# Kernel optimization log

Measured on AMD Instinct MI355X. Metric: run time of the kernel, lower is better.

## Reference

```python
import jax, jax.numpy as jnp
import numpy as np

B, H, N, M, C = 64, 8, 16384, 64, 1024
IVH = 3 * M + 6  # per-head interface size: k(M), beta, g, s(3), gamma, e(M), a(M)


def setup_inputs() -> dict:
    key = jax.random.key(0)
    k1, k2, k3, k4 = jax.random.split(key, 4)
    return {
        "x": jax.random.normal(k1, (B, C), dtype=jnp.float32),
        "current_memory": jax.random.normal(k2, (B, N, M), dtype=jnp.float32),
        "w_prev": jax.random.uniform(k3, (B, H, N), dtype=jnp.float32),
        "W": jax.random.normal(k4, (C, H * IVH), dtype=jnp.float32) * (1.0 / np.sqrt(C)),
        "b": jnp.zeros((H * IVH,), dtype=jnp.float32),
    }


def reference(x, current_memory, w_prev, W, b):
    eps = 1e-16
    iv = (x @ W + b).reshape(B, H, IVH)
    k = iv[..., :M]                                   # [B,H,M] content key
    beta = jax.nn.softplus(iv[..., M])                # [B,H] key strength
    g = jax.nn.sigmoid(iv[..., M + 1])                # [B,H] interpolation gate
    s = jax.nn.softmax(iv[..., M + 2:M + 5], axis=-1) # [B,H,3] shift weights
    gamma = 1.0 + jax.nn.softplus(iv[..., M + 5])     # [B,H] sharpening
    e = jax.nn.sigmoid(iv[..., M + 6:2 * M + 6])      # [B,H,M] erase
    a = iv[..., 2 * M + 6:3 * M + 6]                  # [B,H,M] add

    # content addressing: cosine similarity of k against every memory row
    num = jnp.einsum('bhm,bnm->bhn', k, current_memory)
    den = (jnp.linalg.norm(k, axis=-1)[..., None]
           * jnp.linalg.norm(current_memory, axis=-1)[:, None, :] + eps)
    cos = num / den                                   # [B,H,N]
    wc = jax.nn.softmax(beta[..., None] * cos, axis=-1)

    # gated interpolation with previous weighting
    wg = g[..., None] * wc + (1.0 - g[..., None]) * w_prev

    # circular conv1d shift with 3-tap kernel (shifts -1, 0, +1)
    ws = (s[..., 0:1] * jnp.roll(wg, 1, axis=-1)
          + s[..., 1:2] * wg
          + s[..., 2:3] * jnp.roll(wg, -1, axis=-1))

    # sharpening (power normalize)
    wp = ws ** gamma[..., None]
    w = wp / (jnp.sum(wp, axis=-1, keepdims=True) + eps)

    # read
    read_data = jnp.einsum('bhn,bnm->bhm', w, current_memory)
    return (read_data, w, e, a)
```

## Files before the change

### kernel.cpp

```cpp
#include <hip/hip_runtime.h>
#include <cstdint>
#include <cstddef>

#define B_    64
#define H_    8
#define N_    16384
#define M_    64
#define C_    1024
#define IVH_  198
#define J_    1584
#define NCHUNK_ 64

__device__ __forceinline__ float softplus_f(float x) {
    return (x > 20.f) ? x : log1pf(__expf(x));
}
__device__ __forceinline__ float sigmoid_f(float x) {
    return 1.f / (1.f + __expf(-x));
}

__global__ __launch_bounds__(64) void k_gemm(const float* __restrict__ x,
                                             const float* __restrict__ W,
                                             float* __restrict__ iv) {
    int lane = threadIdx.x;
    int j = blockIdx.x * 64 + lane;
    bool valid = (j < J_);
    int b0 = blockIdx.y * 16;
    int c0 = blockIdx.z * 128;
    const float* xb = x + (size_t)b0 * C_;
    float acc[16];
    #pragma unroll
    for (int i = 0; i < 16; ++i) acc[i] = 0.f;
    #pragma unroll 2
    for (int c = c0; c < c0 + 128; ++c) {
        float wv = valid ? W[(size_t)c * J_ + j] : 0.f;
        #pragma unroll
        for (int bi = 0; bi < 16; ++bi)
            acc[bi] = fmaf(xb[(size_t)bi * C_ + c], wv, acc[bi]);
    }
    if (valid) {
        #pragma unroll
        for (int bi = 0; bi < 16; ++bi)
            atomicAdd(&iv[(size_t)(b0 + bi) * J_ + j], acc[bi]);
    }
}

__global__ void k_params(const float* __restrict__ iv, const float* __restrict__ bias,
                         float* __restrict__ kbuf, float* __restrict__ P,
                         float* __restrict__ out_e, float* __restrict__ out_a) {
    int bh = blockIdx.x;
    int m  = threadIdx.x;
    int b = bh >> 3, h = bh & 7;
    const float* row = iv + (size_t)b * J_ + h * IVH_;
    const float* bb  = bias + h * IVH_;
    float kv = row[m] + bb[m];
    kbuf[(size_t)bh * 64 + m] = kv;
    float s = kv * kv;
    #pragma unroll
    for (int o = 32; o > 0; o >>= 1) s += __shfl_down(s, o, 64);
    float ev = row[70 + m] + bb[70 + m];
    out_e[(size_t)bh * 64 + m] = sigmoid_f(ev);
    out_a[(size_t)bh * 64 + m] = row[134 + m] + bb[134 + m];
    if (m == 0) {
        float knorm = sqrtf(s);
        float v0 = row[64] + bb[64];
        float v1 = row[65] + bb[65];
        float v2 = row[66] + bb[66];
        float v3 = row[67] + bb[67];
        float v4 = row[68] + bb[68];
        float v5 = row[69] + bb[69];
        float beta = softplus_f(v0);
        float g = sigmoid_f(v1);
        float mx = fmaxf(v2, fmaxf(v3, v4));
        float e2 = __expf(v2 - mx), e3 = __expf(v3 - mx), e4 = __expf(v4 - mx);
        float inv = 1.f / (e2 + e3 + e4);
        float gamma = 1.f + softplus_f(v5);
        float* p = P + (size_t)bh * 8;
        p[0] = knorm; p[1] = beta; p[2] = g;
        p[3] = e2 * inv; p[4] = e3 * inv; p[5] = e4 * inv;
        p[6] = gamma;
    }
}

__global__ __launch_bounds__(256, 4) void k_passA(
        const float* __restrict__ mem, const float* __restrict__ kbuf,
        const float* __restrict__ P, float* __restrict__ z,
        float* __restrict__ pmax, float* __restrict__ psum) {
    __shared__ float zl[8 * 257];
    int t = threadIdx.x;
    int b = blockIdx.y;
    int n0 = blockIdx.x << 8;
    int w = t >> 6, lane = t & 63, sub = lane >> 4, mq = lane & 15;

    float4 kreg[8];
    #pragma unroll
    for (int h = 0; h < 8; ++h)
        kreg[h] = *(const float4*)(kbuf + (((size_t)b * 8 + h) << 6) + mq * 4);
    float beta = 0.f, knorm = 1.f;
    if (mq < 8) {
        const float* p = P + (((size_t)b * 8 + mq) << 3);
        knorm = p[0]; beta = p[1];
    }
    const float* mb = mem + ((size_t)b * N_ + n0) * M_;

    #pragma unroll
    for (int rr = 0; rr < 16; ++rr) {
        int row = (w << 6) + (rr << 2) + sub;
        float4 mv = *(const float4*)(mb + (size_t)row * M_ + mq * 4);
        float pr[9];
        #pragma unroll
        for (int h = 0; h < 8; ++h)
            pr[h] = kreg[h].x * mv.x + kreg[h].y * mv.y
                  + kreg[h].z * mv.z + kreg[h].w * mv.w;
        pr[8] = mv.x * mv.x + mv.y * mv.y + mv.z * mv.z + mv.w * mv.w;
        #pragma unroll
        for (int o = 1; o < 16; o <<= 1) {
            #pragma unroll
            for (int i = 0; i < 9; ++i) pr[i] += __shfl_xor(pr[i], o, 64);
        }
        if (mq < 8) {
            float rn = sqrtf(pr[8]);
            zl[mq * 257 + row] = beta * pr[mq] / (knorm * rn + 1e-16f);
        }
    }
    __syncthreads();

    #pragma unroll
    for (int h = 0; h < 8; ++h)
        z[(((size_t)b * 8 + h) << 14) + n0 + t] = zl[h * 257 + t];

    #pragma unroll
    for (int q = 0; q < 2; ++q) {
        int h = w * 2 + q;
        float a0 = zl[h * 257 + lane],       a1 = zl[h * 257 + lane + 64];
        float a2 = zl[h * 257 + lane + 128], a3 = zl[h * 257 + lane + 192];
        float mx = fmaxf(fmaxf(a0, a1), fmaxf(a2, a3));
        #pragma unroll
        for (int o = 32; o > 0; o >>= 1) mx = fmaxf(mx, __shfl_down(mx, o, 64));
        mx = __shfl(mx, 0, 64);
        float se = __expf(a0 - mx) + __expf(a1 - mx) + __expf(a2 - mx) + __expf(a3 - mx);
        #pragma unroll
        for (int o = 32; o > 0; o >>= 1) se += __shfl_down(se, o, 64);
        if (lane == 0) {
            pmax[(((size_t)b * 8 + h) << 6) + blockIdx.x] = mx;
            psum[(((size_t)b * 8 + h) << 6) + blockIdx.x] = se;
        }
    }
}

__global__ void k_stats(const float* __restrict__ pmax, const float* __restrict__ psum,
                        float* __restrict__ stats) {
    int bh = blockIdx.x * 4 + (threadIdx.x >> 6);
    int lane = threadIdx.x & 63;
    float m = pmax[((size_t)bh << 6) + lane];
    float s = psum[((size_t)bh << 6) + lane];
    float mx = m;
    #pragma unroll
    for (int o = 32; o > 0; o >>= 1) mx = fmaxf(mx, __shfl_down(mx, o, 64));
    mx = __shfl(mx, 0, 64);
    float sc = s * __expf(m - mx);
    #pragma unroll
    for (int o = 32; o > 0; o >>= 1) sc += __shfl_down(sc, o, 64);
    if (lane == 0) { stats[bh * 2] = mx; stats[bh * 2 + 1] = 1.f / sc; }
}

__global__ __launch_bounds__(256, 4) void k_passB(
        const float* __restrict__ mem, const float* __restrict__ z,
        const float* __restrict__ wprev, const float* __restrict__ P,
        const float* __restrict__ stats, float* __restrict__ out_w,
        float* __restrict__ sumwp, float* __restrict__ readAcc) {
    __shared__ float smem[3072 + 2064 + 32];
    float* wp_s  = smem;
    float* wgl   = smem + 3072;
    float* racc2 = smem + 3072;
    float* sums  = smem + 3072 + 2064;

    int t = threadIdx.x;
    int b = blockIdx.y;
    int n0 = blockIdx.x << 8;
    int n = n0 + t;
    int w = t >> 6, lane = t & 63, sub = lane >> 4, mq = lane & 15;

    #pragma unroll
    for (int h = 0; h < 8; ++h) {
        size_t bh = (size_t)b * 8 + h;
        float Mx = stats[bh * 2], iS = stats[bh * 2 + 1];
        float g = P[bh * 8 + 2];
        float wc = __expf(z[(bh << 14) + n] - Mx) * iS;
        wgl[h * 258 + t + 1] = fmaf(g, wc, (1.f - g) * wprev[(bh << 14) + n]);
    }
    if (t < 2) {
        int nh   = (t == 0) ? ((n0 + N_ - 1) & (N_ - 1)) : ((n0 + 256) & (N_ - 1));
        int slot = (t == 0) ? 0 : 257;
        #pragma unroll
        for (int h = 0; h < 8; ++h) {
            size_t bh = (size_t)b * 8 + h;
            float Mx = stats[bh * 2], iS = stats[bh * 2 + 1];
            float g = P[bh * 8 + 2];
            float wc = __expf(z[(bh << 14) + nh] - Mx) * iS;
            wgl[h * 258 + slot] = fmaf(g, wc, (1.f - g) * wprev[(bh << 14) + nh]);
        }
    }
    __syncthreads();

    float wpv[8];
    #pragma unroll
    for (int h = 0; h < 8; ++h) {
        size_t bh = (size_t)b * 8 + h;
        float s0 = P[bh * 8 + 3], s1 = P[bh * 8 + 4], s2 = P[bh * 8 + 5];
        float gam = P[bh * 8 + 6];
        float wsv = s0 * wgl[h * 258 + t] + s1 * wgl[h * 258 + t + 1]
                  + s2 * wgl[h * 258 + t + 2];
        float v = __powf(wsv, gam);
        wpv[h] = v;
        out_w[(bh << 14) + n] = v;
    }
    #pragma unroll
    for (int h = 0; h < 8; ++h) {
        float s = wpv[h];
        #pragma unroll
        for (int o = 32; o > 0; o >>= 1) s += __shfl_down(s, o, 64);
        if (lane == 0) sums[w * 8 + h] = s;
    }
    *(float4*)(wp_s + t * 12)     = make_float4(wpv[0], wpv[1], wpv[2], wpv[3]);
    *(float4*)(wp_s + t * 12 + 4) = make_float4(wpv[4], wpv[5], wpv[6], wpv[7]);
    __syncthreads();
    if (t < 8)
        atomicAdd(&sumwp[b * 8 + t], sums[t] + sums[8 + t] + sums[16 + t] + sums[24 + t]);

    float4 acc[8];
    #pragma unroll
    for (int h = 0; h < 8; ++h) acc[h] = make_float4(0.f, 0.f, 0.f, 0.f);
    const float* mb = mem + ((size_t)b * N_ + n0) * M_;
    #pragma unroll
    for (int rr = 0; rr < 16; ++rr) {
        int row = (w << 6) + (rr << 2) + sub;
        float4 mv = *(const float4*)(mb + (size_t)row * M_ + mq * 4);
        float4 wA = *(const float4*)(wp_s + row * 12);
        float4 wB = *(const float4*)(wp_s + row * 12 + 4);
        float wv8[8] = {wA.x, wA.y, wA.z, wA.w, wB.x, wB.y, wB.z, wB.w};
        #pragma unroll
        for (int h = 0; h < 8; ++h) {
            acc[h].x = fmaf(wv8[h], mv.x, acc[h].x);
            acc[h].y = fmaf(wv8[h], mv.y, acc[h].y);
            acc[h].z = fmaf(wv8[h], mv.z, acc[h].z);
            acc[h].w = fmaf(wv8[h], mv.w, acc[h].w);
        }
    }
    #pragma unroll
    for (int h = 0; h < 8; ++h) {
        #pragma unroll
        for (int o = 32; o >= 16; o >>= 1) {
            acc[h].x += __shfl_down(acc[h].x, o, 64);
            acc[h].y += __shfl_down(acc[h].y, o, 64);
            acc[h].z += __shfl_down(acc[h].z, o, 64);
            acc[h].w += __shfl_down(acc[h].w, o, 64);
        }
    }
    if (lane < 16) {
        #pragma unroll
        for (int h = 0; h < 8; ++h)
            *(float4*)(racc2 + ((w * 8 + h) << 6) + mq * 4) = acc[h];
    }
    __syncthreads();
    #pragma unroll
    for (int r = 0; r < 2; ++r) {
        int idx = r * 256 + t;
        float s = racc2[idx] + racc2[512 + idx] + racc2[1024 + idx] + racc2[1536 + idx];
        atomicAdd(&readAcc[(size_t)b * 512 + idx], s);
    }
}

__global__ void k_norm(float* __restrict__ out_w, const float* __restrict__ sumwp) {
    size_t idx = (size_t)blockIdx.x * 256 + threadIdx.x;
    int bh = (int)((idx * 4) >> 14);
    float inv = 1.f / (sumwp[bh] + 1e-16f);
    float4* p = (float4*)out_w + idx;
    float4 v = *p;
    v.x *= inv; v.y *= inv; v.z *= inv; v.w *= inv;
    *p = v;
}

__global__ void k_read(const float* __restrict__ readAcc, const float* __restrict__ sumwp,
                       float* __restrict__ out_rd) {
    int i = blockIdx.x * 256 + threadIdx.x;
    int bh = i >> 6;
    out_rd[i] = readAcc[i] / (sumwp[bh] + 1e-16f);
}

extern "C" void kernel_launch(void* const* d_in, const int* in_sizes, int n_in,
                              void* d_out, int out_size, void* d_ws, size_t ws_size,
                              hipStream_t stream) {
    const float* x     = (const float*)d_in[0];
    const float* mem   = (const float*)d_in[1];
    const float* wprev = (const float*)d_in[2];
    const float* W     = (const float*)d_in[3];
    const float* bias  = (const float*)d_in[4];

    float* out   = (float*)d_out;
    float* out_rd = out;
    float* out_w  = out + 32768;
    float* out_e  = out + 32768 + 8388608;
    float* out_a  = out_e + 32768;

    float* ws     = (float*)d_ws;
    float* iv      = ws;
    float* kbuf    = iv + 101376;
    float* P       = kbuf + 32768;
    float* zbuf    = P + 4096;
    float* pmax    = zbuf + 8388608;
    float* psum    = pmax + 32768;
    float* stats   = psum + 32768;
    float* sumwp   = stats + 1024;
    float* readAcc = sumwp + 512;

    hipMemsetAsync(iv, 0, (size_t)101376 * 4, stream);
    hipMemsetAsync(sumwp, 0, (size_t)(512 + 32768) * 4, stream);

    k_gemm  <<<dim3(25, 4, 8), 64, 0, stream>>>(x, W, iv);
    k_params<<<512, 64, 0, stream>>>(iv, bias, kbuf, P, out_e, out_a);
    k_passA <<<dim3(NCHUNK_, B_), 256, 0, stream>>>(mem, kbuf, P, zbuf, pmax, psum);
    k_stats <<<128, 256, 0, stream>>>(pmax, psum, stats);
    k_passB <<<dim3(NCHUNK_, B_), 256, 0, stream>>>(mem, zbuf, wprev, P, stats,
                                                    out_w, sumwp, readAcc);
    k_norm  <<<8192, 256, 0, stream>>>(out_w, sumwp);
    k_read  <<<128, 256, 0, stream>>>(readAcc, sumwp, out_rd);
}
```

Measured before the change: 540.4 us.

## Process batch in groups so memory tile stays cache-resident between passes

Splits the passA/stats/passB/norm sequence into four launches over groups of 16 batches, so the memory slice and z buffer read by passB (and out_w read by norm) were touched recently and may still be in the last-level cache. It also splits the GEMM reduction dimension into 16 chunks instead of 8 to launch more blocks. The cost is four times as many kernel launches with smaller grids, and more atomic adds in the GEMM.

```diff
diff --git a/kernel.cpp b/kernel.cpp
--- a/kernel.cpp
+++ b/kernel.cpp
@@ -10,6 +10,7 @@
 #define IVH_  198
 #define J_    1584
 #define NCHUNK_ 64
+#define BGRP_  16
 
 __device__ __forceinline__ float softplus_f(float x) {
     return (x > 20.f) ? x : log1pf(__expf(x));
@@ -25,13 +26,13 @@
     int j = blockIdx.x * 64 + lane;
     bool valid = (j < J_);
     int b0 = blockIdx.y * 16;
-    int c0 = blockIdx.z * 128;
+    int c0 = blockIdx.z * 64;
     const float* xb = x + (size_t)b0 * C_;
     float acc[16];
     #pragma unroll
     for (int i = 0; i < 16; ++i) acc[i] = 0.f;
     #pragma unroll 2
-    for (int c = c0; c < c0 + 128; ++c) {
+    for (int c = c0; c < c0 + 64; ++c) {
         float wv = valid ? W[(size_t)c * J_ + j] : 0.f;
         #pragma unroll
         for (int bi = 0; bi < 16; ++bi)
@@ -84,10 +85,10 @@
 __global__ __launch_bounds__(256, 4) void k_passA(
         const float* __restrict__ mem, const float* __restrict__ kbuf,
         const float* __restrict__ P, float* __restrict__ z,
-        float* __restrict__ pmax, float* __restrict__ psum) {
+        float* __restrict__ pmax, float* __restrict__ psum, int b0g) {
     __shared__ float zl[8 * 257];
     int t = threadIdx.x;
-    int b = blockIdx.y;
+    int b = b0g + blockIdx.y;
     int n0 = blockIdx.x << 8;
     int w = t >> 6, lane = t & 63, sub = lane >> 4, mq = lane & 15;
 
@@ -148,8 +149,8 @@
 }
 
 __global__ void k_stats(const float* __restrict__ pmax, const float* __restrict__ psum,
-                        float* __restrict__ stats) {
-    int bh = blockIdx.x * 4 + (threadIdx.x >> 6);
+                        float* __restrict__ stats, int bh0) {
+    int bh = bh0 + blockIdx.x * 4 + (threadIdx.x >> 6);
     int lane = threadIdx.x & 63;
     float m = pmax[((size_t)bh << 6) + lane];
     float s = psum[((size_t)bh << 6) + lane];
@@ -167,7 +168,7 @@
         const float* __restrict__ mem, const float* __restrict__ z,
         const float* __restrict__ wprev, const float* __restrict__ P,
         const float* __restrict__ stats, float* __restrict__ out_w,
-        float* __restrict__ sumwp, float* __restrict__ readAcc) {
+        float* __restrict__ sumwp, float* __restrict__ readAcc, int b0g) {
     __shared__ float smem[3072 + 2064 + 32];
     float* wp_s  = smem;
     float* wgl   = smem + 3072;
@@ -175,7 +176,7 @@
     float* sums  = smem + 3072 + 2064;
 
     int t = threadIdx.x;
-    int b = blockIdx.y;
+    int b = b0g + blockIdx.y;
     int n0 = blockIdx.x << 8;
     int n = n0 + t;
     int w = t >> 6, lane = t & 63, sub = lane >> 4, mq = lane & 15;
@@ -270,8 +271,10 @@
     }
 }
 
-__global__ void k_norm(float* __restrict__ out_w, const float* __restrict__ sumwp) {
-    size_t idx = (size_t)blockIdx.x * 256 + threadIdx.x;
+__global__ void k_norm(float* __restrict__ out_w, const float* __restrict__ sumwp,
+                       int bh0) {
+    size_t base = ((size_t)bh0 << 14) >> 2;
+    size_t idx = base + (size_t)blockIdx.x * 256 + threadIdx.x;
     int bh = (int)((idx * 4) >> 14);
     float inv = 1.f / (sumwp[bh] + 1e-16f);
     float4* p = (float4*)out_w + idx;
@@ -316,12 +319,18 @@
     hipMemsetAsync(iv, 0, (size_t)101376 * 4, stream);
     hipMemsetAsync(sumwp, 0, (size_t)(512 + 32768) * 4, stream);
 
-    k_gemm  <<<dim3(25, 4, 8), 64, 0, stream>>>(x, W, iv);
+    k_gemm  <<<dim3(25, 4, 16), 64, 0, stream>>>(x, W, iv);
     k_params<<<512, 64, 0, stream>>>(iv, bias, kbuf, P, out_e, out_a);
-    k_passA <<<dim3(NCHUNK_, B_), 256, 0, stream>>>(mem, kbuf, P, zbuf, pmax, psum);
-    k_stats <<<128, 256, 0, stream>>>(pmax, psum, stats);
-    k_passB <<<dim3(NCHUNK_, B_), 256, 0, stream>>>(mem, zbuf, wprev, P, stats,
-                                                    out_w, sumwp, readAcc);
-    k_norm  <<<8192, 256, 0, stream>>>(out_w, sumwp);
+
+    for (int g = 0; g < B_ / BGRP_; ++g) {
+        int b0  = g * BGRP_;
+        int bh0 = b0 * 8;
+        k_passA<<<dim3(NCHUNK_, BGRP_), 256, 0, stream>>>(mem, kbuf, P, zbuf,
+                                                          pmax, psum, b0);
+        k_stats<<<32, 256, 0, stream>>>(pmax, psum, stats, bh0);
+        k_passB<<<dim3(NCHUNK_, BGRP_), 256, 0, stream>>>(mem, zbuf, wprev, P, stats,
+                                                          out_w, sumwp, readAcc, b0);
+        k_norm <<<2048, 256, 0, stream>>>(out_w, sumwp, bh0);
+    }
     k_read  <<<128, 256, 0, stream>>>(readAcc, sumwp, out_rd);
 }
```

Measured after the change: 587.0 us. 8.6% more time.

## Fuse attention passes into one cooperative kernel with LDS-resident weights

Applied to the files above, without the earlier changes.

Merges passA, stats, passB, normalization and the read finalization into a single cooperative kernel. Each block now owns a 1024-row segment and keeps its logits and weights in LDS across grid-wide syncs. This removes the global z round-trip, the separate normalization pass over out_w, the extra launches and the memsets; buffer zeroing now happens inside the kernel. The projection GEMM also drops split-K atomics in favour of full-K blocks covering 4 batch rows each. The trade-offs are much heavier LDS use per block, cooperative-launch residency requirements, grid-sync stalls, and more repeated W reads in the GEMM.

```diff
diff --git a/kernel.cpp b/kernel.cpp
--- a/kernel.cpp
+++ b/kernel.cpp
@@ -1,6 +1,9 @@
 #include <hip/hip_runtime.h>
+#include <hip/hip_cooperative_groups.h>
 #include <cstdint>
 #include <cstddef>
+
+namespace cg = cooperative_groups;
 
 #define B_    64
 #define H_    8
@@ -9,7 +12,8 @@
 #define C_    1024
 #define IVH_  198
 #define J_    1584
-#define NCHUNK_ 64
+#define NSEG_ 16
+#define SEGROWS_ 1024
 
 __device__ __forceinline__ float softplus_f(float x) {
     return (x > 20.f) ? x : log1pf(__expf(x));
@@ -24,23 +28,22 @@
     int lane = threadIdx.x;
     int j = blockIdx.x * 64 + lane;
     bool valid = (j < J_);
-    int b0 = blockIdx.y * 16;
-    int c0 = blockIdx.z * 128;
+    int b0 = blockIdx.y * 4;
     const float* xb = x + (size_t)b0 * C_;
-    float acc[16];
-    #pragma unroll
-    for (int i = 0; i < 16; ++i) acc[i] = 0.f;
-    #pragma unroll 2
-    for (int c = c0; c < c0 + 128; ++c) {
+    float a0 = 0.f, a1 = 0.f, a2 = 0.f, a3 = 0.f;
+    #pragma unroll 4
+    for (int c = 0; c < C_; ++c) {
         float wv = valid ? W[(size_t)c * J_ + j] : 0.f;
-        #pragma unroll
-        for (int bi = 0; bi < 16; ++bi)
-            acc[bi] = fmaf(xb[(size_t)bi * C_ + c], wv, acc[bi]);
+        a0 = fmaf(xb[c],           wv, a0);
+        a1 = fmaf(xb[C_ + c],      wv, a1);
+        a2 = fmaf(xb[2 * C_ + c],  wv, a2);
+        a3 = fmaf(xb[3 * C_ + c],  wv, a3);
     }
     if (valid) {
-        #pragma unroll
-        for (int bi = 0; bi < 16; ++bi)
-            atomicAdd(&iv[(size_t)(b0 + bi) * J_ + j], acc[bi]);
+        iv[(size_t)(b0 + 0) * J_ + j] = a0;
+        iv[(size_t)(b0 + 1) * J_ + j] = a1;
+        iv[(size_t)(b0 + 2) * J_ + j] = a2;
+        iv[(size_t)(b0 + 3) * J_ + j] = a3;
     }
 }
 
@@ -81,15 +84,30 @@
     }
 }
 
-__global__ __launch_bounds__(256, 4) void k_passA(
+__global__ __launch_bounds__(256, 4) void k_fused(
         const float* __restrict__ mem, const float* __restrict__ kbuf,
-        const float* __restrict__ P, float* __restrict__ z,
-        float* __restrict__ pmax, float* __restrict__ psum) {
-    __shared__ float zl[8 * 257];
+        const float* __restrict__ P, const float* __restrict__ wprev,
+        float* __restrict__ z_bound, float* __restrict__ pmax,
+        float* __restrict__ psum, float* __restrict__ sumwp,
+        float* __restrict__ readAcc, float* __restrict__ out_w,
+        float* __restrict__ out_rd) {
+    __shared__ float z_lds[8 * 1028];
+    __shared__ float pbuf[64];
+    __shared__ float sM[8], sIS[8];
+    __shared__ float wg_ext[16];
+    __shared__ float edge_wg[8];
+    __shared__ float sums[32];
+
     int t = threadIdx.x;
-    int b = blockIdx.y;
-    int n0 = blockIdx.x << 8;
+    int blk = blockIdx.x;
+    int b = blk >> 4, seg = blk & 15;
     int w = t >> 6, lane = t & 63, sub = lane >> 4, mq = lane & 15;
+    int n0 = seg * SEGROWS_;
+
+    if (blk < 130) {
+        int idx = blk * 256 + t;
+        if (idx < 33280) sumwp[idx] = 0.f;
+    }
 
     float4 kreg[8];
     #pragma unroll
@@ -103,126 +121,141 @@
     const float* mb = mem + ((size_t)b * N_ + n0) * M_;
 
     #pragma unroll
-    for (int rr = 0; rr < 16; ++rr) {
-        int row = (w << 6) + (rr << 2) + sub;
-        float4 mv = *(const float4*)(mb + (size_t)row * M_ + mq * 4);
-        float pr[9];
-        #pragma unroll
-        for (int h = 0; h < 8; ++h)
-            pr[h] = kreg[h].x * mv.x + kreg[h].y * mv.y
-                  + kreg[h].z * mv.z + kreg[h].w * mv.w;
-        pr[8] = mv.x * mv.x + mv.y * mv.y + mv.z * mv.z + mv.w * mv.w;
-        #pragma unroll
-        for (int o = 1; o < 16; o <<= 1) {
+    for (int ch = 0; ch < 4; ++ch) {
+        #pragma unroll
+        for (int rr = 0; rr < 16; ++rr) {
+            int rl = ch * 256 + (w << 6) + (rr << 2) + sub;
+            float4 mv = *(const float4*)(mb + (size_t)rl * M_ + mq * 4);
+            float pr[9];
             #pragma unroll
-            for (int i = 0; i < 9; ++i) pr[i] += __shfl_xor(pr[i], o, 64);
-        }
-        if (mq < 8) {
-            float rn = sqrtf(pr[8]);
-            zl[mq * 257 + row] = beta * pr[mq] / (knorm * rn + 1e-16f);
+            for (int h = 0; h < 8; ++h)
+                pr[h] = kreg[h].x * mv.x + kreg[h].y * mv.y
+                      + kreg[h].z * mv.z + kreg[h].w * mv.w;
+            pr[8] = mv.x * mv.x + mv.y * mv.y + mv.z * mv.z + mv.w * mv.w;
+            #pragma unroll
+            for (int o = 1; o < 16; o <<= 1) {
+                #pragma unroll
+                for (int i = 0; i < 9; ++i) pr[i] += __shfl_xor(pr[i], o, 64);
+            }
+            if (mq < 8) {
+                float rn = sqrtf(pr[8]);
+                z_lds[mq * 1028 + rl] = beta * pr[mq] / (knorm * rn + 1e-16f);
+            }
         }
     }
     __syncthreads();
 
-    #pragma unroll
-    for (int h = 0; h < 8; ++h)
-        z[(((size_t)b * 8 + h) << 14) + n0 + t] = zl[h * 257 + t];
+    if (t < 16) {
+        int side = t >> 3, h = t & 7;
+        z_bound[((size_t)(b * 16 + seg) * 2 + side) * 8 + h] =
+            z_lds[h * 1028 + (side ? (SEGROWS_ - 1) : 0)];
+    }
 
     #pragma unroll
     for (int q = 0; q < 2; ++q) {
         int h = w * 2 + q;
-        float a0 = zl[h * 257 + lane],       a1 = zl[h * 257 + lane + 64];
-        float a2 = zl[h * 257 + lane + 128], a3 = zl[h * 257 + lane + 192];
-        float mx = fmaxf(fmaxf(a0, a1), fmaxf(a2, a3));
+        float v[16];
+        #pragma unroll
+        for (int i = 0; i < 16; ++i) v[i] = z_lds[h * 1028 + lane + i * 64];
+        float mx = v[0];
+        #pragma unroll
+        for (int i = 1; i < 16; ++i) mx = fmaxf(mx, v[i]);
         #pragma unroll
         for (int o = 32; o > 0; o >>= 1) mx = fmaxf(mx, __shfl_down(mx, o, 64));
         mx = __shfl(mx, 0, 64);
-        float se = __expf(a0 - mx) + __expf(a1 - mx) + __expf(a2 - mx) + __expf(a3 - mx);
+        float se = 0.f;
+        #pragma unroll
+        for (int i = 0; i < 16; ++i) se += __expf(v[i] - mx);
         #pragma unroll
         for (int o = 32; o > 0; o >>= 1) se += __shfl_down(se, o, 64);
         if (lane == 0) {
-            pmax[(((size_t)b * 8 + h) << 6) + blockIdx.x] = mx;
-            psum[(((size_t)b * 8 + h) << 6) + blockIdx.x] = se;
-        }
-    }
-}
-
-__global__ void k_stats(const float* __restrict__ pmax, const float* __restrict__ psum,
-                        float* __restrict__ stats) {
-    int bh = blockIdx.x * 4 + (threadIdx.x >> 6);
-    int lane = threadIdx.x & 63;
-    float m = pmax[((size_t)bh << 6) + lane];
-    float s = psum[((size_t)bh << 6) + lane];
-    float mx = m;
-    #pragma unroll
-    for (int o = 32; o > 0; o >>= 1) mx = fmaxf(mx, __shfl_down(mx, o, 64));
-    mx = __shfl(mx, 0, 64);
-    float sc = s * __expf(m - mx);
-    #pragma unroll
-    for (int o = 32; o > 0; o >>= 1) sc += __shfl_down(sc, o, 64);
-    if (lane == 0) { stats[bh * 2] = mx; stats[bh * 2 + 1] = 1.f / sc; }
-}
-
-__global__ __launch_bounds__(256, 4) void k_passB(
-        const float* __restrict__ mem, const float* __restrict__ z,
-        const float* __restrict__ wprev, const float* __restrict__ P,
-        const float* __restrict__ stats, float* __restrict__ out_w,
-        float* __restrict__ sumwp, float* __restrict__ readAcc) {
-    __shared__ float smem[3072 + 2064 + 32];
-    float* wp_s  = smem;
-    float* wgl   = smem + 3072;
-    float* racc2 = smem + 3072;
-    float* sums  = smem + 3072 + 2064;
-
-    int t = threadIdx.x;
-    int b = blockIdx.y;
-    int n0 = blockIdx.x << 8;
-    int n = n0 + t;
-    int w = t >> 6, lane = t & 63, sub = lane >> 4, mq = lane & 15;
+            pmax[(size_t)(b * 8 + h) * 16 + seg] = mx;
+            psum[(size_t)(b * 8 + h) * 16 + seg] = se;
+        }
+    }
+
+    cg::this_grid().sync();
+
+    if (t < 8) {
+        int h = t;
+        const float* pm = pmax + (size_t)(b * 8 + h) * 16;
+        const float* ps = psum + (size_t)(b * 8 + h) * 16;
+        float mx = pm[0];
+        #pragma unroll
+        for (int i = 1; i < 16; ++i) mx = fmaxf(mx, pm[i]);
+        float s = 0.f;
+        #pragma unroll
+        for (int i = 0; i < 16; ++i) s += ps[i] * __expf(pm[i] - mx);
+        sM[h] = mx; sIS[h] = 1.f / s;
+    }
+    if (t < 64) pbuf[t] = P[(size_t)b * 64 + t];
+    __syncthreads();
+
+    if (t < 16) {
+        int side = t >> 3, h = t & 7;
+        int nbseg = side ? ((seg + 1) & 15) : ((seg + 15) & 15);
+        float zb = z_bound[((size_t)(b * 16 + nbseg) * 2 + (side ? 0 : 1)) * 8 + h];
+        int nbrow = side ? ((n0 + SEGROWS_) & (N_ - 1)) : ((n0 - 1) & (N_ - 1));
+        float g = pbuf[h * 8 + 2];
+        float wc = __expf(zb - sM[h]) * sIS[h];
+        wg_ext[side * 8 + h] =
+            fmaf(g, wc, (1.f - g) * wprev[(((size_t)(b * 8 + h)) << 14) + nbrow]);
+    }
+
+    #pragma unroll
+    for (int it = 0; it < 4; ++it) {
+        int rl = it * 256 + t;
+        int n = n0 + rl;
+        #pragma unroll
+        for (int h = 0; h < 8; ++h) {
+            float g = pbuf[h * 8 + 2];
+            float wc = __expf(z_lds[h * 1028 + rl] - sM[h]) * sIS[h];
+            float wpr = wprev[(((size_t)(b * 8 + h)) << 14) + n];
+            z_lds[h * 1028 + rl] = fmaf(g, wc, (1.f - g) * wpr);
+        }
+    }
+    __syncthreads();
+
+    float swp[8];
+    #pragma unroll
+    for (int h = 0; h < 8; ++h) swp[h] = 0.f;
+    for (int it = 0; it < 4; ++it) {
+        int rl = it * 256 + t;
+        float wmv[8], wpv[8];
+        #pragma unroll
+        for (int h = 0; h < 8; ++h) {
+            float wl;
+            if (rl == 0)          wl = wg_ext[h];
+            else if (t == 0)      wl = edge_wg[h];
+            else                  wl = z_lds[h * 1028 + rl - 1];
+            float wr = (rl == SEGROWS_ - 1) ? wg_ext[8 + h]
+                                            : z_lds[h * 1028 + rl + 1];
+            float wm = z_lds[h * 1028 + rl];
+            wmv[h] = wm;
+            float s0 = pbuf[h * 8 + 3], s1 = pbuf[h * 8 + 4], s2 = pbuf[h * 8 + 5];
+            float gam = pbuf[h * 8 + 6];
+            float wsv = s0 * wl + s1 * wm + s2 * wr;
+            float v = __powf(wsv, gam);
+            wpv[h] = v;
+            swp[h] += v;
+        }
+        __syncthreads();
+        if (t == 255) {
+            #pragma unroll
+            for (int h = 0; h < 8; ++h) edge_wg[h] = wmv[h];
+        }
+        #pragma unroll
+        for (int h = 0; h < 8; ++h) z_lds[h * 1028 + rl] = wpv[h];
+        __syncthreads();
+    }
 
     #pragma unroll
     for (int h = 0; h < 8; ++h) {
-        size_t bh = (size_t)b * 8 + h;
-        float Mx = stats[bh * 2], iS = stats[bh * 2 + 1];
-        float g = P[bh * 8 + 2];
-        float wc = __expf(z[(bh << 14) + n] - Mx) * iS;
-        wgl[h * 258 + t + 1] = fmaf(g, wc, (1.f - g) * wprev[(bh << 14) + n]);
-    }
-    if (t < 2) {
-        int nh   = (t == 0) ? ((n0 + N_ - 1) & (N_ - 1)) : ((n0 + 256) & (N_ - 1));
-        int slot = (t == 0) ? 0 : 257;
-        #pragma unroll
-        for (int h = 0; h < 8; ++h) {
-            size_t bh = (size_t)b * 8 + h;
-            float Mx = stats[bh * 2], iS = stats[bh * 2 + 1];
-            float g = P[bh * 8 + 2];
-            float wc = __expf(z[(bh << 14) + nh] - Mx) * iS;
-            wgl[h * 258 + slot] = fmaf(g, wc, (1.f - g) * wprev[(bh << 14) + nh]);
-        }
-    }
-    __syncthreads();
-
-    float wpv[8];
-    #pragma unroll
-    for (int h = 0; h < 8; ++h) {
-        size_t bh = (size_t)b * 8 + h;
-        float s0 = P[bh * 8 + 3], s1 = P[bh * 8 + 4], s2 = P[bh * 8 + 5];
-        float gam = P[bh * 8 + 6];
-        float wsv = s0 * wgl[h * 258 + t] + s1 * wgl[h * 258 + t + 1]
-                  + s2 * wgl[h * 258 + t + 2];
-        float v = __powf(wsv, gam);
-        wpv[h] = v;
-        out_w[(bh << 14) + n] = v;
-    }
-    #pragma unroll
-    for (int h = 0; h < 8; ++h) {
-        float s = wpv[h];
+        float s = swp[h];
         #pragma unroll
         for (int o = 32; o > 0; o >>= 1) s += __shfl_down(s, o, 64);
         if (lane == 0) sums[w * 8 + h] = s;
     }
-    *(float4*)(wp_s + t * 12)     = make_float4(wpv[0], wpv[1], wpv[2], wpv[3]);
-    *(float4*)(wp_s + t * 12 + 4) = make_float4(wpv[4], wpv[5], wpv[6], wpv[7]);
     __syncthreads();
     if (t < 8)
         atomicAdd(&sumwp[b * 8 + t], sums[t] + sums[8 + t] + sums[16 + t] + sums[24 + t]);
@@ -230,20 +263,20 @@
     float4 acc[8];
     #pragma unroll
     for (int h = 0; h < 8; ++h) acc[h] = make_float4(0.f, 0.f, 0.f, 0.f);
-    const float* mb = mem + ((size_t)b * N_ + n0) * M_;
-    #pragma unroll
-    for (int rr = 0; rr < 16; ++rr) {
-        int row = (w << 6) + (rr << 2) + sub;
-        float4 mv = *(const float4*)(mb + (size_t)row * M_ + mq * 4);
-        float4 wA = *(const float4*)(wp_s + row * 12);
-        float4 wB = *(const float4*)(wp_s + row * 12 + 4);
-        float wv8[8] = {wA.x, wA.y, wA.z, wA.w, wB.x, wB.y, wB.z, wB.w};
-        #pragma unroll
-        for (int h = 0; h < 8; ++h) {
-            acc[h].x = fmaf(wv8[h], mv.x, acc[h].x);
-            acc[h].y = fmaf(wv8[h], mv.y, acc[h].y);
-            acc[h].z = fmaf(wv8[h], mv.z, acc[h].z);
-            acc[h].w = fmaf(wv8[h], mv.w, acc[h].w);
+    #pragma unroll
+    for (int ch = 0; ch < 4; ++ch) {
+        #pragma unroll
+        for (int rr = 0; rr < 16; ++rr) {
+            int rl = ch * 256 + (w << 6) + (rr << 2) + sub;
+            float4 mv = *(const float4*)(mb + (size_t)rl * M_ + mq * 4);
+            #pragma unroll
+            for (int h = 0; h < 8; ++h) {
+                float wv = z_lds[h * 1028 + rl];
+                acc[h].x = fmaf(wv, mv.x, acc[h].x);
+                acc[h].y = fmaf(wv, mv.y, acc[h].y);
+                acc[h].z = fmaf(wv, mv.z, acc[h].z);
+                acc[h].w = fmaf(wv, mv.w, acc[h].w);
+            }
         }
     }
     #pragma unroll
@@ -258,33 +291,36 @@
     }
     if (lane < 16) {
         #pragma unroll
+        for (int h = 0; h < 8; ++h) {
+            float* dst = readAcc + (size_t)b * 512 + h * 64 + mq * 4;
+            atomicAdd(dst + 0, acc[h].x);
+            atomicAdd(dst + 1, acc[h].y);
+            atomicAdd(dst + 2, acc[h].z);
+            atomicAdd(dst + 3, acc[h].w);
+        }
+    }
+
+    cg::this_grid().sync();
+
+    float inv[8];
+    #pragma unroll
+    for (int h = 0; h < 8; ++h) inv[h] = 1.f / (sumwp[b * 8 + h] + 1e-16f);
+    #pragma unroll
+    for (int it = 0; it < 4; ++it) {
+        int rl = it * 256 + t;
+        int n = n0 + rl;
+        #pragma unroll
         for (int h = 0; h < 8; ++h)
-            *(float4*)(racc2 + ((w * 8 + h) << 6) + mq * 4) = acc[h];
-    }
-    __syncthreads();
-    #pragma unroll
-    for (int r = 0; r < 2; ++r) {
-        int idx = r * 256 + t;
-        float s = racc2[idx] + racc2[512 + idx] + racc2[1024 + idx] + racc2[1536 + idx];
-        atomicAdd(&readAcc[(size_t)b * 512 + idx], s);
-    }
-}
-
-__global__ void k_norm(float* __restrict__ out_w, const float* __restrict__ sumwp) {
-    size_t idx = (size_t)blockIdx.x * 256 + threadIdx.x;
-    int bh = (int)((idx * 4) >> 14);
-    float inv = 1.f / (sumwp[bh] + 1e-16f);
-    float4* p = (float4*)out_w + idx;
-    float4 v = *p;
-    v.x *= inv; v.y *= inv; v.z *= inv; v.w *= inv;
-    *p = v;
-}
-
-__global__ void k_read(const float* __restrict__ readAcc, const float* __restrict__ sumwp,
-                       float* __restrict__ out_rd) {
-    int i = blockIdx.x * 256 + threadIdx.x;
-    int bh = i >> 6;
-    out_rd[i] = readAcc[i] / (sumwp[bh] + 1e-16f);
+            out_w[(((size_t)(b * 8 + h)) << 14) + n] = z_lds[h * 1028 + rl] * inv[h];
+    }
+    if (seg == 0) {
+        #pragma unroll
+        for (int r = 0; r < 2; ++r) {
+            int idx = r * 256 + t;
+            out_rd[(size_t)b * 512 + idx] =
+                readAcc[(size_t)b * 512 + idx] * inv[idx >> 6];
+        }
+    }
 }
 
 extern "C" void kernel_launch(void* const* d_in, const int* in_sizes, int n_in,
@@ -296,32 +332,30 @@
     const float* W     = (const float*)d_in[3];
     const float* bias  = (const float*)d_in[4];
 
-    float* out   = (float*)d_out;
+    float* out    = (float*)d_out;
     float* out_rd = out;
     float* out_w  = out + 32768;
     float* out_e  = out + 32768 + 8388608;
     float* out_a  = out_e + 32768;
 
-    float* ws     = (float*)d_ws;
+    float* ws      = (float*)d_ws;
     float* iv      = ws;
     float* kbuf    = iv + 101376;
     float* P       = kbuf + 32768;
-    float* zbuf    = P + 4096;
-    float* pmax    = zbuf + 8388608;
-    float* psum    = pmax + 32768;
-    float* stats   = psum + 32768;
-    float* sumwp   = stats + 1024;
+    float* z_bound = P + 4096;
+    float* pmax    = z_bound + 16384;
+    float* psum    = pmax + 8192;
+    float* sumwp   = psum + 8192;
     float* readAcc = sumwp + 512;
 
-    hipMemsetAsync(iv, 0, (size_t)101376 * 4, stream);
-    hipMemsetAsync(sumwp, 0, (size_t)(512 + 32768) * 4, stream);
-
-    k_gemm  <<<dim3(25, 4, 8), 64, 0, stream>>>(x, W, iv);
+    k_gemm  <<<dim3(25, 16), 64, 0, stream>>>(x, W, iv);
     k_params<<<512, 64, 0, stream>>>(iv, bias, kbuf, P, out_e, out_a);
-    k_passA <<<dim3(NCHUNK_, B_), 256, 0, stream>>>(mem, kbuf, P, zbuf, pmax, psum);
-    k_stats <<<128, 256, 0, stream>>>(pmax, psum, stats);
-    k_passB <<<dim3(NCHUNK_, B_), 256, 0, stream>>>(mem, zbuf, wprev, P, stats,
-                                                    out_w, sumwp, readAcc);
-    k_norm  <<<8192, 256, 0, stream>>>(out_w, sumwp);
-    k_read  <<<128, 256, 0, stream>>>(readAcc, sumwp, out_rd);
-}
+
+    void* args[] = {
+        (void*)&mem, (void*)&kbuf, (void*)&P, (void*)&wprev,
+        (void*)&z_bound, (void*)&pmax, (void*)&psum, (void*)&sumwp,
+        (void*)&readAcc, (void*)&out_w, (void*)&out_rd
+    };
+    hipLaunchCooperativeKernel((void*)k_fused, dim3(1024), dim3(256),
+                               args, 0, stream);
+}
```

Measured after the change: 902.4 us. 1.67x slower.
